# Optimization experiments

Measured on AMD Instinct MI355X. Metric: run time of the kernel, lower is better.

Reference implementation:

```python
import jax, jax.numpy as jnp
import numpy as np

B, N, M, C, H = 4, 2048, 2048, 1024, 16
D = C // H  # head_dim = 64
SCALE = D ** -0.5


def setup_inputs() -> dict:
    key = jax.random.key(0)
    ks = jax.random.split(key, 8)
    std = C ** -0.5
    return {
        "query": jax.random.normal(ks[0], (B, N, C), jnp.float32),
        "key": jax.random.normal(ks[1], (B, M, C), jnp.float32),
        "value": jax.random.normal(ks[2], (B, M, C), jnp.float32),
        "Wq": jax.random.normal(ks[3], (C, C), jnp.float32) * std,
        "Wk": jax.random.normal(ks[4], (C, C), jnp.float32) * std,
        "Wv": jax.random.normal(ks[5], (C, C), jnp.float32) * std,
        "Wp": jax.random.normal(ks[6], (C, C), jnp.float32) * std,
        "bp": jax.random.normal(ks[7], (C,), jnp.float32) * 0.01,
    }


def reference(query, key, value, Wq, Wk, Wv, Wp, bp):
    # Linear: y = x @ W.T (torch nn.Linear convention), no bias for q/k/v.
    # reshape (B,S,C)->(B,S,H,D)->(B,H,S,D)
    q = jnp.einsum('bnc,dc->bnd', query, Wq).reshape(B, N, H, D).transpose(0, 2, 1, 3)
    k = jnp.einsum('bmc,dc->bmd', key, Wk).reshape(B, M, H, D).transpose(0, 2, 1, 3)
    v = jnp.einsum('bmc,dc->bmd', value, Wv).reshape(B, M, H, D).transpose(0, 2, 1, 3)
    # scaled scores, softmax over keys
    attn = jnp.einsum('bhnd,bhmd->bhnm', q * SCALE, k)
    attn = jax.nn.softmax(attn, axis=-1)
    # attention output -> (B,N,C)
    x = jnp.einsum('bhnm,bhmd->bhnd', attn, v).transpose(0, 2, 1, 3).reshape(B, N, C)
    # output projection with bias
    return jnp.einsum('bnc,dc->bnd', x, Wp) + bp
```

## Files before the change

kernel.cpp:

```cpp
#include <hip/hip_runtime.h>
#include <stdint.h>

#define B_ 4
#define N_ 2048
#define M_ 2048
#define C_ 1024
#define H_ 16
#define D_ 64
#define SC_ (B_*N_*C_)
#define CC_ (C_*C_)

typedef unsigned short u16;
typedef __attribute__((ext_vector_type(8))) short short8;
typedef __attribute__((ext_vector_type(4))) short short4v;
typedef __attribute__((ext_vector_type(4))) float f32x4;

#if __has_builtin(__builtin_amdgcn_exp2f)
#define EXP2F __builtin_amdgcn_exp2f
#else
#define EXP2F exp2f
#endif

__device__ inline u16 f2bf(float f) {
    union { float f; uint32_t u; } v; v.f = f;
    uint32_t r = v.u + 0x7fffu + ((v.u >> 16) & 1u);
    return (u16)(r >> 16);
}

__device__ inline f32x4 mfma16x16x16_bf16(short4v a, short4v b, f32x4 c) {
#if __has_builtin(__builtin_amdgcn_mfma_f32_16x16x16bf16_1k)
    return __builtin_amdgcn_mfma_f32_16x16x16bf16_1k(a, b, c, 0, 0, 0);
#else
    asm volatile("v_mfma_f32_16x16x16_bf16 %0, %1, %2, %0"
                 : "+v"(c) : "v"(a), "v"(b));
    return c;
#endif
}

__global__ __launch_bounds__(256) void convert_kernel(
    const float* __restrict__ q, const float* __restrict__ k, const float* __restrict__ v,
    const float* __restrict__ wq, const float* __restrict__ wk,
    const float* __restrict__ wv, const float* __restrict__ wp,
    u16* __restrict__ qf, u16* __restrict__ kf, u16* __restrict__ vf,
    u16* __restrict__ wqb, u16* __restrict__ wkb, u16* __restrict__ wvb, u16* __restrict__ wpb)
{
    const int SC4 = SC_ / 4;
    const int CC4 = CC_ / 4;
    const int total = 3 * SC4 + 4 * CC4;
    for (int i = blockIdx.x * 256 + threadIdx.x; i < total; i += gridDim.x * 256) {
        const float* src; u16* dst; int off;
        if (i < 3 * SC4) {
            int seg = i >> 21;
            off = (i & (SC4 - 1)) << 2;
            src = seg == 0 ? q : seg == 1 ? k : v;
            dst = seg == 0 ? qf : seg == 1 ? kf : vf;
        } else {
            int j = i - 3 * SC4;
            int seg = j >> 18;
            off = (j & (CC4 - 1)) << 2;
            src = seg == 0 ? wq : seg == 1 ? wk : seg == 2 ? wv : wp;
            dst = seg == 0 ? wqb : seg == 1 ? wkb : seg == 2 ? wvb : wpb;
        }
        float4 val = *(const float4*)(src + off);
        ushort4 h;
        h.x = f2bf(val.x); h.y = f2bf(val.y); h.z = f2bf(val.z); h.w = f2bf(val.w);
        *(ushort4*)(dst + off) = h;
    }
}

template<int OMODE>
__global__ __launch_bounds__(256) void gemm_lds(
    const u16* __restrict__ A, const u16* __restrict__ Wb,
    const float* __restrict__ bias, void* __restrict__ Op, float scale)
{
    const int K = 1024;
    __shared__ u16 SH[2 * 8192];
    const int tid = threadIdx.x;
    const int wid = tid >> 6, lane = tid & 63;
    const int quad = lane >> 4, l15 = lane & 15;
    const int f = blockIdx.x;
    const int m0 = (f & 63) * 128, n0 = (f >> 6) * 128;
    const int wm = (wid >> 1) * 64, wn = (wid & 1) * 64;

    size_t aoff[2], boff[2];
    int dsto[2];
#pragma unroll
    for (int i = 0; i < 2; ++i) {
        int s = tid + i * 256;
        int row = s >> 2, c8 = (s & 3) << 3;
        aoff[i] = (size_t)(m0 + row) * K + c8;
        boff[i] = (size_t)(n0 + row) * K + c8;
        dsto[i] = s * 8;
    }

    f32x4 acc[4][4];
#pragma unroll
    for (int i = 0; i < 4; ++i)
#pragma unroll
        for (int j = 0; j < 4; ++j) acc[i][j] = f32x4{0.f, 0.f, 0.f, 0.f};

#pragma unroll
    for (int i = 0; i < 2; ++i) {
        __builtin_amdgcn_global_load_lds(
            (const __attribute__((address_space(1))) void*)(A + aoff[i]),
            (__attribute__((address_space(3))) void*)(SH + dsto[i]), 16, 0, 0);
        __builtin_amdgcn_global_load_lds(
            (const __attribute__((address_space(1))) void*)(Wb + boff[i]),
            (__attribute__((address_space(3))) void*)(SH + 4096 + dsto[i]), 16, 0, 0);
    }

    for (int it = 0; it < 32; ++it) {
        const int cur = (it & 1) * 8192;
        __syncthreads();
        if (it + 1 < 32) {
            const int nxt = ((it + 1) & 1) * 8192;
            const int k0n = (it + 1) * 32;
#pragma unroll
            for (int i = 0; i < 2; ++i) {
                __builtin_amdgcn_global_load_lds(
                    (const __attribute__((address_space(1))) void*)(A + aoff[i] + k0n),
                    (__attribute__((address_space(3))) void*)(SH + nxt + dsto[i]), 16, 0, 0);
                __builtin_amdgcn_global_load_lds(
                    (const __attribute__((address_space(1))) void*)(Wb + boff[i] + k0n),
                    (__attribute__((address_space(3))) void*)(SH + nxt + 4096 + dsto[i]), 16, 0, 0);
            }
        }
        short8 av[4], bv[4];
#pragma unroll
        for (int i = 0; i < 4; ++i)
            av[i] = *(const short8*)(SH + cur + (wm + i * 16 + l15) * 32 + quad * 8);
#pragma unroll
        for (int j = 0; j < 4; ++j)
            bv[j] = *(const short8*)(SH + cur + 4096 + (wn + j * 16 + l15) * 32 + quad * 8);
#pragma unroll
        for (int i = 0; i < 4; ++i)
#pragma unroll
            for (int j = 0; j < 4; ++j)
                acc[i][j] = __builtin_amdgcn_mfma_f32_16x16x32_bf16(av[i], bv[j], acc[i][j], 0, 0, 0);
    }

    if (OMODE == 2) {
#pragma unroll
        for (int j = 0; j < 4; ++j) {
            int col = n0 + wn + j * 16 + l15;
            float bb = bias[col];
#pragma unroll
            for (int i = 0; i < 4; ++i) {
                int row = m0 + wm + i * 16 + quad * 4;
#pragma unroll
                for (int r = 0; r < 4; ++r)
                    ((float*)Op)[(size_t)(row + r) * 1024 + col] = acc[i][j][r] * scale + bb;
            }
        }
    } else if (OMODE == 0) {
#pragma unroll
        for (int j = 0; j < 4; ++j) {
            int col = n0 + wn + j * 16 + l15;
#pragma unroll
            for (int i = 0; i < 4; ++i) {
                int row = m0 + wm + i * 16 + quad * 4;
#pragma unroll
                for (int r = 0; r < 4; ++r)
                    ((u16*)Op)[(size_t)(row + r) * 1024 + col] = f2bf(acc[i][j][r] * scale);
            }
        }
    } else {
#pragma unroll
        for (int j = 0; j < 4; ++j) {
            int col = n0 + wn + j * 16 + l15;
            int hh = col >> 6, dd = col & 63;
#pragma unroll
            for (int i = 0; i < 4; ++i) {
                int row = m0 + wm + i * 16 + quad * 4;
                int bb = row >> 11, mm = row & 2047;
                ushort4 hv;
                hv.x = f2bf(acc[i][j][0] * scale);
                hv.y = f2bf(acc[i][j][1] * scale);
                hv.z = f2bf(acc[i][j][2] * scale);
                hv.w = f2bf(acc[i][j][3] * scale);
                *(ushort4*)((u16*)Op + (((size_t)bb * 16 + hh) * 64 + dd) * 2048 + mm) = hv;
            }
        }
    }
}

__global__ __launch_bounds__(256, 3) void attn_kernel(
    const u16* __restrict__ qg, const u16* __restrict__ kg,
    const u16* __restrict__ vT, u16* __restrict__ xb)
{
    __shared__ __align__(16) char smem[32768];
    u16* KV = (u16*)smem;
    float* Ored = (float*)smem;
    float* Lred = (float*)(smem + 16384);

    const int tid = threadIdx.x;
    const int wid = tid >> 6, lane = tid & 63;
    const int quad = lane >> 4, l15 = lane & 15;
    const int f = blockIdx.x;
    const int bh = f & 63, qt = f >> 6;
    const int b = bh >> 4, h = bh & 15;

    const u16* qbase = qg + ((size_t)(b * N_ + qt * 64)) * C_ + h * 64;
    short8 qf[4][2];
#pragma unroll
    for (int qb2 = 0; qb2 < 4; ++qb2)
#pragma unroll
        for (int ch = 0; ch < 2; ++ch)
            qf[qb2][ch] = *(const short8*)(qbase + (size_t)(qb2 * 16 + l15) * C_ + ch * 32 + quad * 8);

    const u16* kptr[2];
    const u16* vptr[2];
    int dsto[2];
#pragma unroll
    for (int i = 0; i < 2; ++i) {
        int s = tid + i * 256;
        int row = s >> 3, g = s & 7;
        int gsw = g ^ (row & 7);
        kptr[i] = kg + ((size_t)(b * M_ + row)) * C_ + h * 64 + gsw * 8;
        vptr[i] = vT + (((size_t)b * 16 + h) * 64 + row) * M_ + gsw * 8;
        dsto[i] = s * 8;
    }

    f32x4 acc_o[4][4];
#pragma unroll
    for (int i = 0; i < 4; ++i)
#pragma unroll
        for (int j = 0; j < 4; ++j) acc_o[i][j] = f32x4{0.f, 0.f, 0.f, 0.f};
    float lsum[4] = {0.f, 0.f, 0.f, 0.f};

    const int rk = wid * 16 + l15, swk = rk & 7;
    const int kfo0 = rk * 64 + ((0 * 4 + quad) ^ swk) * 8;
    const int kfo1 = rk * 64 + ((1 * 4 + quad) ^ swk) * 8;
    int vfo[4];
#pragma unroll
    for (int db = 0; db < 4; ++db) {
        int rv = db * 16 + l15, swv = rv & 7;
        vfo[db] = 4096 + rv * 64 + (((wid * 2 + (quad >> 1)) ^ swv) << 3) + ((quad & 1) << 2);
    }

    union { short4v s; uint32_t u[2]; } pfrag[4], vfu;

#pragma unroll
    for (int i = 0; i < 2; ++i) {
        __builtin_amdgcn_global_load_lds(
            (const __attribute__((address_space(1))) void*)(kptr[i]),
            (__attribute__((address_space(3))) void*)(KV + dsto[i]), 16, 0, 0);
        __builtin_amdgcn_global_load_lds(
            (const __attribute__((address_space(1))) void*)(vptr[i]),
            (__attribute__((address_space(3))) void*)(KV + 4096 + dsto[i]), 16, 0, 0);
    }

    for (int it = 0; it < 32; ++it) {
        const int cur = (it & 1) * 8192;
        __syncthreads();
        if (it + 1 < 32) {
            const int nxt = ((it + 1) & 1) * 8192;
            const int kvn = (it + 1) * 64;
#pragma unroll
            for (int i = 0; i < 2; ++i) {
                __builtin_amdgcn_global_load_lds(
                    (const __attribute__((address_space(1))) void*)(kptr[i] + (size_t)kvn * C_),
                    (__attribute__((address_space(3))) void*)(KV + nxt + dsto[i]), 16, 0, 0);
                __builtin_amdgcn_global_load_lds(
                    (const __attribute__((address_space(1))) void*)(vptr[i] + kvn),
                    (__attribute__((address_space(3))) void*)(KV + nxt + 4096 + dsto[i]), 16, 0, 0);
            }
        }

        short8 kf0 = *(const short8*)(KV + cur + kfo0);
        short8 kf1 = *(const short8*)(KV + cur + kfo1);
        f32x4 sc[4];
#pragma unroll
        for (int qb2 = 0; qb2 < 4; ++qb2) {
            sc[qb2] = f32x4{0.f, 0.f, 0.f, 0.f};
            sc[qb2] = __builtin_amdgcn_mfma_f32_16x16x32_bf16(kf0, qf[qb2][0], sc[qb2], 0, 0, 0);
            sc[qb2] = __builtin_amdgcn_mfma_f32_16x16x32_bf16(kf1, qf[qb2][1], sc[qb2], 0, 0, 0);
        }

#pragma unroll
        for (int qb2 = 0; qb2 < 4; ++qb2) {
            float e0 = EXP2F(sc[qb2][0]);
            float e1 = EXP2F(sc[qb2][1]);
            float e2 = EXP2F(sc[qb2][2]);
            float e3 = EXP2F(sc[qb2][3]);
            lsum[qb2] += (e0 + e1) + (e2 + e3);
            pfrag[qb2].u[0] = __builtin_amdgcn_perm(__builtin_bit_cast(uint32_t, e1),
                                                    __builtin_bit_cast(uint32_t, e0), 0x07060302u);
            pfrag[qb2].u[1] = __builtin_amdgcn_perm(__builtin_bit_cast(uint32_t, e3),
                                                    __builtin_bit_cast(uint32_t, e2), 0x07060302u);
        }

#pragma unroll
        for (int db = 0; db < 4; ++db) {
            uint2 vlo = *(const uint2*)(KV + cur + vfo[db]);
            vfu.u[0] = vlo.x; vfu.u[1] = vlo.y;
#pragma unroll
            for (int qb2 = 0; qb2 < 4; ++qb2)
                acc_o[qb2][db] = mfma16x16x16_bf16(vfu.s, pfrag[qb2].s, acc_o[qb2][db]);
        }
    }

    __syncthreads();
    *(f32x4*)(Lred + (((wid * 4 + quad) * 16 + l15) << 2)) =
        f32x4{lsum[0], lsum[1], lsum[2], lsum[3]};
    __syncthreads();
    float dsum = 0.f;
#pragma unroll
    for (int q2 = 0; q2 < 4; ++q2)
        dsum += Lred[(((quad * 4 + q2) * 16 + l15) << 2) + wid];
    dsum += __shfl_xor(dsum, 16);
    dsum += __shfl_xor(dsum, 32);
    float dinv = 1.f / dsum;

#pragma unroll
    for (int qb2 = 0; qb2 < 4; ++qb2) {
        __syncthreads();
#pragma unroll
        for (int db = 0; db < 4; ++db)
            *(f32x4*)(Ored + (((wid * 4 + db) * 64 + lane) << 2)) = acc_o[qb2][db];
        __syncthreads();
        if (wid == qb2) {
#pragma unroll
            for (int w2 = 0; w2 < 4; ++w2) {
                if (w2 == wid) continue;
#pragma unroll
                for (int db = 0; db < 4; ++db) {
                    f32x4 t = *(const f32x4*)(Ored + (((w2 * 4 + db) * 64 + lane) << 2));
                    acc_o[qb2][db] += t;
                }
            }
            size_t ob = ((size_t)(b * N_ + qt * 64 + wid * 16 + l15)) * C_ + h * 64;
#pragma unroll
            for (int db = 0; db < 4; ++db) {
                ushort4 st;
                st.x = f2bf(acc_o[qb2][db][0] * dinv);
                st.y = f2bf(acc_o[qb2][db][1] * dinv);
                st.z = f2bf(acc_o[qb2][db][2] * dinv);
                st.w = f2bf(acc_o[qb2][db][3] * dinv);
                *(ushort4*)(xb + ob + db * 16 + quad * 4) = st;
            }
        }
    }
}

extern "C" void kernel_launch(void* const* d_in, const int* in_sizes, int n_in,
                              void* d_out, int out_size, void* d_ws, size_t ws_size,
                              hipStream_t stream) {
    const float* query = (const float*)d_in[0];
    const float* key   = (const float*)d_in[1];
    const float* value = (const float*)d_in[2];
    const float* Wq    = (const float*)d_in[3];
    const float* Wk    = (const float*)d_in[4];
    const float* Wv    = (const float*)d_in[5];
    const float* Wpm   = (const float*)d_in[6];
    const float* bp    = (const float*)d_in[7];
    float* out = (float*)d_out;

    u16* base = (u16*)d_ws;
    u16* qf  = base;
    u16* kf  = base + (size_t)SC_;
    u16* vf  = base + (size_t)2 * SC_;
    u16* kb  = base + (size_t)3 * SC_;
    u16* Wqb = base + (size_t)4 * SC_;
    u16* Wkb = Wqb + CC_;
    u16* Wvb = Wkb + CC_;
    u16* Wpb = Wvb + CC_;
    u16* vTp = kf;
    u16* qb  = vf;
    u16* xb  = qf;

    hipLaunchKernelGGL(convert_kernel, dim3(4096), dim3(256), 0, stream,
                       query, key, value, Wq, Wk, Wv, Wpm,
                       qf, kf, vf, Wqb, Wkb, Wvb, Wpb);

    dim3 gg(512), bb(256);
    hipLaunchKernelGGL((gemm_lds<0>), gg, bb, 0, stream, kf, Wkb, nullptr, (void*)kb, 1.0f);
    hipLaunchKernelGGL((gemm_lds<1>), gg, bb, 0, stream, vf, Wvb, nullptr, (void*)vTp, 1.0f);
    hipLaunchKernelGGL((gemm_lds<0>), gg, bb, 0, stream, qf, Wqb, nullptr, (void*)qb,
                       0.125f * 1.44269504088896340736f);

    hipLaunchKernelGGL(attn_kernel, dim3(2048), bb, 0, stream, qb, kb, vTp, xb);

    hipLaunchKernelGGL((gemm_lds<2>), gg, bb, 0, stream, xb, Wpb, bp, (void*)out, 1.0f);
}
```

Measured before the change: 367.2 us.

## Triple-buffer LDS tiles with partial vmcnt waits in GEMM and attention

Result: faster. 339.9 us (-7.4%).

```diff
diff --git a/kernel.cpp b/kernel.cpp
--- a/kernel.cpp
+++ b/kernel.cpp
@@ -36,6 +36,13 @@
     return c;
 #endif
 }
+
+#define WAIT_BARRIER(N)                                         \
+    do {                                                        \
+        asm volatile("s_waitcnt vmcnt(" #N ")" ::: "memory");   \
+        __builtin_amdgcn_s_barrier();                           \
+        __builtin_amdgcn_sched_barrier(0);                      \
+    } while (0)
 
 __global__ __launch_bounds__(256) void convert_kernel(
     const float* __restrict__ q, const float* __restrict__ k, const float* __restrict__ v,
@@ -74,7 +81,7 @@
     const float* __restrict__ bias, void* __restrict__ Op, float scale)
 {
     const int K = 1024;
-    __shared__ u16 SH[2 * 8192];
+    __shared__ u16 SH[3 * 8192];
     const int tid = threadIdx.x;
     const int wid = tid >> 6, lane = tid & 63;
     const int quad = lane >> 4, l15 = lane & 15;
@@ -100,21 +107,26 @@
         for (int j = 0; j < 4; ++j) acc[i][j] = f32x4{0.f, 0.f, 0.f, 0.f};
 
 #pragma unroll
-    for (int i = 0; i < 2; ++i) {
-        __builtin_amdgcn_global_load_lds(
-            (const __attribute__((address_space(1))) void*)(A + aoff[i]),
-            (__attribute__((address_space(3))) void*)(SH + dsto[i]), 16, 0, 0);
-        __builtin_amdgcn_global_load_lds(
-            (const __attribute__((address_space(1))) void*)(Wb + boff[i]),
-            (__attribute__((address_space(3))) void*)(SH + 4096 + dsto[i]), 16, 0, 0);
+    for (int t = 0; t < 2; ++t) {
+        const int bo = t * 8192, k0 = t * 32;
+#pragma unroll
+        for (int i = 0; i < 2; ++i) {
+            __builtin_amdgcn_global_load_lds(
+                (const __attribute__((address_space(1))) void*)(A + aoff[i] + k0),
+                (__attribute__((address_space(3))) void*)(SH + bo + dsto[i]), 16, 0, 0);
+            __builtin_amdgcn_global_load_lds(
+                (const __attribute__((address_space(1))) void*)(Wb + boff[i] + k0),
+                (__attribute__((address_space(3))) void*)(SH + bo + 4096 + dsto[i]), 16, 0, 0);
+        }
     }
 
     for (int it = 0; it < 32; ++it) {
-        const int cur = (it & 1) * 8192;
-        __syncthreads();
-        if (it + 1 < 32) {
-            const int nxt = ((it + 1) & 1) * 8192;
-            const int k0n = (it + 1) * 32;
+        const int cur = (it % 3) * 8192;
+        if (it < 31) WAIT_BARRIER(4);
+        else         WAIT_BARRIER(0);
+        if (it + 2 < 32) {
+            const int nxt = ((it + 2) % 3) * 8192;
+            const int k0n = (it + 2) * 32;
 #pragma unroll
             for (int i = 0; i < 2; ++i) {
                 __builtin_amdgcn_global_load_lds(
@@ -188,7 +200,7 @@
     const u16* __restrict__ qg, const u16* __restrict__ kg,
     const u16* __restrict__ vT, u16* __restrict__ xb)
 {
-    __shared__ __align__(16) char smem[32768];
+    __shared__ __align__(16) char smem[49152];
     u16* KV = (u16*)smem;
     float* Ored = (float*)smem;
     float* Lred = (float*)(smem + 16384);
@@ -241,21 +253,26 @@
     union { short4v s; uint32_t u[2]; } pfrag[4], vfu;
 
 #pragma unroll
-    for (int i = 0; i < 2; ++i) {
-        __builtin_amdgcn_global_load_lds(
-            (const __attribute__((address_space(1))) void*)(kptr[i]),
-            (__attribute__((address_space(3))) void*)(KV + dsto[i]), 16, 0, 0);
-        __builtin_amdgcn_global_load_lds(
-            (const __attribute__((address_space(1))) void*)(vptr[i]),
-            (__attribute__((address_space(3))) void*)(KV + 4096 + dsto[i]), 16, 0, 0);
+    for (int t = 0; t < 2; ++t) {
+        const int bo = t * 8192, kv0 = t * 64;
+#pragma unroll
+        for (int i = 0; i < 2; ++i) {
+            __builtin_amdgcn_global_load_lds(
+                (const __attribute__((address_space(1))) void*)(kptr[i] + (size_t)kv0 * C_),
+                (__attribute__((address_space(3))) void*)(KV + bo + dsto[i]), 16, 0, 0);
+            __builtin_amdgcn_global_load_lds(
+                (const __attribute__((address_space(1))) void*)(vptr[i] + kv0),
+                (__attribute__((address_space(3))) void*)(KV + bo + 4096 + dsto[i]), 16, 0, 0);
+        }
     }
 
     for (int it = 0; it < 32; ++it) {
-        const int cur = (it & 1) * 8192;
-        __syncthreads();
-        if (it + 1 < 32) {
-            const int nxt = ((it + 1) & 1) * 8192;
-            const int kvn = (it + 1) * 64;
+        const int cur = (it % 3) * 8192;
+        if (it < 31) WAIT_BARRIER(4);
+        else         WAIT_BARRIER(0);
+        if (it + 2 < 32) {
+            const int nxt = ((it + 2) % 3) * 8192;
+            const int kvn = (it + 2) * 64;
 #pragma unroll
             for (int i = 0; i < 2; ++i) {
                 __builtin_amdgcn_global_load_lds(
```
